# Kernel tuning notes

Hardware: AMD Instinct MI355X
Metric: run time of the kernel (lower is better)

## Reference

```python
import jax, jax.numpy as jnp
import numpy as np

NUM_EXPERTS_TOTAL = 9  # 8 routed + 1 shared (shared expert is also routed via softmax in this module)
TOP_K = 2


def setup_inputs() -> dict:
    key = jax.random.key(0)
    k0, k1, k2, k3, k4 = jax.random.split(key, 5)
    B, S, H, I = 2, 2048, 1024, 2816
    E = NUM_EXPERTS_TOTAL
    x = jax.random.normal(k0, (B, S, H), dtype=jnp.float32)
    Wr = (jax.random.normal(k1, (H, E), dtype=jnp.float32) * 0.02)          # router (no bias)
    Wg = (jax.random.normal(k2, (E, H, I), dtype=jnp.float32) * 0.02)       # gate_proj per expert
    Wu = (jax.random.normal(k3, (E, H, I), dtype=jnp.float32) * 0.02)       # up_proj per expert
    Wd = (jax.random.normal(k4, (E, I, H), dtype=jnp.float32) * 0.02)       # down_proj per expert
    return {"x": x, "Wr": Wr, "Wg": Wg, "Wu": Wu, "Wd": Wd}


def reference(x, Wr, Wg, Wu, Wd):
    B, S, H = x.shape
    E = NUM_EXPERTS_TOTAL
    T = B * S

    # Router: softmax over all 9 experts, then top-2 and renormalize
    logits = jnp.einsum('bsh,he->bse', x, Wr)
    probs = jax.nn.softmax(logits, axis=-1)
    topk_w, topk_idx = jax.lax.top_k(probs, TOP_K)                 # [B,S,K]
    topk_w = topk_w / jnp.sum(topk_w, axis=-1, keepdims=True)

    xf = x.reshape(T, H)
    wf = topk_w.reshape(T, TOP_K)
    idxf = topk_idx.reshape(T, TOP_K)

    # Per-token combine weight for each expert (0 if not selected)
    cw = jnp.zeros((T, E), dtype=x.dtype).at[jnp.arange(T)[:, None], idxf].add(wf)  # [T,E]

    # SwiGLU MLP for every expert (tokens with cw==0 contribute nothing)
    gate = jax.nn.silu(jnp.einsum('th,ehi->tei', xf, Wg))          # [T,E,I]
    hidden = gate * jnp.einsum('th,ehi->tei', xf, Wu)              # [T,E,I]
    out = jnp.einsum('tei,eih,te->th', hidden, Wd, cw)             # weighted combine
    return out.reshape(B, S, H)
```

## Files before the change

kernel.cpp:

```cpp
#include <hip/hip_runtime.h>
#include <cstdint>
#include <cstddef>

#define T_TOK 4096
#define H_DIM 1024
#define I_DIM 2816
#define E_NUM 9
#define MAXTILE 76

typedef __bf16 bf16;
typedef bf16 bf16x4 __attribute__((ext_vector_type(4)));
typedef bf16 bf16x8 __attribute__((ext_vector_type(8)));
typedef float f32x4 __attribute__((ext_vector_type(4)));

constexpr int BM = 128, BN = 128, BK = 32;

#define GL16(gp, lp)                                                                   \
  __builtin_amdgcn_global_load_lds((const __attribute__((address_space(1))) void*)(gp), \
                                   (__attribute__((address_space(3))) void*)(lp), 16, 0, 0)

__global__ __launch_bounds__(256) void k_xcast(const float* __restrict__ x, bf16* __restrict__ xb) {
  size_t i = ((size_t)blockIdx.x * 256 + threadIdx.x) * 8;
  float4 a = *reinterpret_cast<const float4*>(x + i);
  float4 b = *reinterpret_cast<const float4*>(x + i + 4);
  bf16x8 v;
  v[0]=(bf16)a.x; v[1]=(bf16)a.y; v[2]=(bf16)a.z; v[3]=(bf16)a.w;
  v[4]=(bf16)b.x; v[5]=(bf16)b.y; v[6]=(bf16)b.z; v[7]=(bf16)b.w;
  *reinterpret_cast<bf16x8*>(xb + i) = v;
}

__global__ __launch_bounds__(256) void k_transpose(const float* __restrict__ in,
                                                   bf16* __restrict__ out, int R, int C) {
  const float* src = in + (size_t)blockIdx.z * R * C;
  bf16* dst = out + (size_t)blockIdx.z * R * C;
  __shared__ bf16 tile[64][72];
  int r0 = blockIdx.y * 64, c0 = blockIdx.x * 64;
  int t = threadIdx.x;
  int tr = t >> 4, tc = (t & 15) * 4;
#pragma unroll
  for (int it = 0; it < 4; ++it) {
    int r = tr + it * 16;
    float4 v = *reinterpret_cast<const float4*>(src + (size_t)(r0 + r) * C + c0 + tc);
    bf16x4 w; w[0]=(bf16)v.x; w[1]=(bf16)v.y; w[2]=(bf16)v.z; w[3]=(bf16)v.w;
    *reinterpret_cast<bf16x4*>(&tile[r][tc]) = w;
  }
  __syncthreads();
#pragma unroll
  for (int it = 0; it < 4; ++it) {
    int oc = tr + it * 16;
    bf16x4 w;
    w[0] = tile[tc + 0][oc]; w[1] = tile[tc + 1][oc];
    w[2] = tile[tc + 2][oc]; w[3] = tile[tc + 3][oc];
    *reinterpret_cast<bf16x4*>(dst + (size_t)(c0 + oc) * R + r0 + tc) = w;
  }
}

__global__ __launch_bounds__(256) void k_router(const float* __restrict__ x,
                                                const float* __restrict__ Wr,
                                                int* __restrict__ ridx,
                                                float* __restrict__ rw,
                                                int* __restrict__ counts) {
  int lane = threadIdx.x & 63;
  int wid  = threadIdx.x >> 6;
  int t = blockIdx.x * 4 + wid;
  const float* xr = x + (size_t)t * H_DIM;
  float acc[E_NUM];
#pragma unroll
  for (int e = 0; e < E_NUM; ++e) acc[e] = 0.f;
  for (int h = lane; h < H_DIM; h += 64) {
    float xv = xr[h];
    const float* wr = Wr + h * E_NUM;
#pragma unroll
    for (int e = 0; e < E_NUM; ++e) acc[e] += xv * wr[e];
  }
#pragma unroll
  for (int off = 32; off > 0; off >>= 1) {
#pragma unroll
    for (int e = 0; e < E_NUM; ++e) acc[e] += __shfl_xor(acc[e], off);
  }
  if (lane == 0) {
    int i0 = 0;
#pragma unroll
    for (int e = 1; e < E_NUM; ++e) if (acc[e] > acc[i0]) i0 = e;
    int i1 = (i0 == 0) ? 1 : 0;
#pragma unroll
    for (int e = 0; e < E_NUM; ++e) if (e != i0 && acc[e] > acc[i1]) i1 = e;
    float r  = expf(acc[i1] - acc[i0]);
    float w0 = 1.f / (1.f + r);
    float w1 = r / (1.f + r);
    ridx[2 * t]     = i0;
    ridx[2 * t + 1] = i1;
    rw[2 * t]     = w0;
    rw[2 * t + 1] = w1;
    atomicAdd(&counts[i0], 1);
    atomicAdd(&counts[i1], 1);
  }
}

__global__ void k_scan(const int* __restrict__ counts, int* __restrict__ offsets,
                       int* __restrict__ cursor, int* __restrict__ tiles,
                       int* __restrict__ n_tiles) {
  if (threadIdx.x == 0) {
    int s = 0, nt = 0;
    for (int e = 0; e < E_NUM; ++e) {
      offsets[e] = s;
      int c = counts[e];
      for (int pt = 0; pt * BM < c && nt < MAXTILE; ++pt) tiles[nt++] = (e << 16) | pt;
      s += c;
    }
    offsets[E_NUM] = s;
    *n_tiles = nt;
  }
  if (threadIdx.x < E_NUM) cursor[threadIdx.x] = 0;
}

__global__ __launch_bounds__(256) void k_scatter(const int* __restrict__ ridx,
                                                 const int* __restrict__ offsets,
                                                 int* __restrict__ cursor,
                                                 int* __restrict__ perm) {
  int t = blockIdx.x * 256 + threadIdx.x;
  if (t >= T_TOK) return;
#pragma unroll
  for (int k = 0; k < 2; ++k) {
    int e = ridx[2 * t + k];
    int pos = atomicAdd(&cursor[e], 1);
    perm[offsets[e] + pos] = 2 * t + k;
  }
}

__global__ __launch_bounds__(256, 2) void k_gateup(const bf16* __restrict__ xb,
                                                   const bf16* __restrict__ WgT,
                                                   const bf16* __restrict__ WuT,
                                                   const int* __restrict__ perm,
                                                   const int* __restrict__ offsets,
                                                   const int* __restrict__ tiles,
                                                   const int* __restrict__ n_tiles,
                                                   bf16* __restrict__ hidden) {
  if ((int)blockIdx.y >= *n_tiles) return;
  int tv = tiles[blockIdx.y];
  int e = tv >> 16, pt = tv & 0xffff;
  int seg0 = offsets[e], cnt = offsets[e + 1] - seg0;
  int n0 = blockIdx.x * BN;

  __shared__ bf16 As[BM * BK];
  __shared__ bf16 Bg[BN * BK];
  __shared__ bf16 Bu[BN * BK];

  int tid = threadIdx.x, lane = tid & 63, wid = tid >> 6;
  int wm = wid >> 1, wn = wid & 1, l15 = lane & 15, l16 = lane >> 4;

  int srow1 = tid >> 2, srow2 = 64 + (tid >> 2);
  int kc = (tid & 3) * 8;
  int p1 = pt * BM + srow1, p2 = pt * BM + srow2;
  const bf16* a1 = xb + (size_t)(perm[seg0 + (p1 < cnt ? p1 : 0)] >> 1) * H_DIM + kc;
  const bf16* a2 = xb + (size_t)(perm[seg0 + (p2 < cnt ? p2 : 0)] >> 1) * H_DIM + kc;
  const bf16* g1 = WgT + ((size_t)e * I_DIM + n0 + srow1) * H_DIM + kc;
  const bf16* g2 = WgT + ((size_t)e * I_DIM + n0 + srow2) * H_DIM + kc;
  const bf16* u1 = WuT + ((size_t)e * I_DIM + n0 + srow1) * H_DIM + kc;
  const bf16* u2 = WuT + ((size_t)e * I_DIM + n0 + srow2) * H_DIM + kc;
  bf16* lA1 = &As[tid * 8];       bf16* lA2 = &As[2048 + tid * 8];
  bf16* lG1 = &Bg[tid * 8];       bf16* lG2 = &Bg[2048 + tid * 8];
  bf16* lU1 = &Bu[tid * 8];       bf16* lU2 = &Bu[2048 + tid * 8];

  f32x4 accg[4][4], accu[4][4];
#pragma unroll
  for (int m = 0; m < 4; ++m)
#pragma unroll
    for (int n = 0; n < 4; ++n) {
      accg[m][n] = (f32x4){0.f, 0.f, 0.f, 0.f};
      accu[m][n] = (f32x4){0.f, 0.f, 0.f, 0.f};
    }

  for (int k0 = 0; k0 < H_DIM; k0 += BK) {
    GL16(a1 + k0, lA1);  GL16(a2 + k0, lA2);
    GL16(g1 + k0, lG1);  GL16(g2 + k0, lG2);
    GL16(u1 + k0, lU1);  GL16(u2 + k0, lU2);
    __syncthreads();

    bf16x8 af[4], bg[4], bu[4];
#pragma unroll
    for (int m = 0; m < 4; ++m)
      af[m] = *reinterpret_cast<const bf16x8*>(&As[(wm * 64 + m * 16 + l15) * BK + l16 * 8]);
#pragma unroll
    for (int n = 0; n < 4; ++n) {
      bg[n] = *reinterpret_cast<const bf16x8*>(&Bg[(wn * 64 + n * 16 + l15) * BK + l16 * 8]);
      bu[n] = *reinterpret_cast<const bf16x8*>(&Bu[(wn * 64 + n * 16 + l15) * BK + l16 * 8]);
    }
#pragma unroll
    for (int m = 0; m < 4; ++m)
#pragma unroll
      for (int n = 0; n < 4; ++n) {
        accg[m][n] = __builtin_amdgcn_mfma_f32_16x16x32_bf16(af[m], bg[n], accg[m][n], 0, 0, 0);
        accu[m][n] = __builtin_amdgcn_mfma_f32_16x16x32_bf16(af[m], bu[n], accu[m][n], 0, 0, 0);
      }
    __syncthreads();
  }

#pragma unroll
  for (int m = 0; m < 4; ++m) {
#pragma unroll
    for (int r = 0; r < 4; ++r) {
      int p_glob = pt * BM + wm * 64 + m * 16 + l16 * 4 + r;
      if (p_glob < cnt) {
        bf16* hrow = hidden + (size_t)(seg0 + p_glob) * I_DIM;
#pragma unroll
        for (int n = 0; n < 4; ++n) {
          int col = n0 + wn * 64 + n * 16 + l15;
          float g = accg[m][n][r];
          float u = accu[m][n][r];
          float h = g / (1.f + __expf(-g)) * u;
          hrow[col] = (bf16)h;
        }
      }
    }
  }
}

__global__ __launch_bounds__(256, 2) void k_down(const bf16* __restrict__ hidden,
                                                 const bf16* __restrict__ WdT,
                                                 const int* __restrict__ perm,
                                                 const int* __restrict__ offsets,
                                                 const int* __restrict__ tiles,
                                                 const int* __restrict__ n_tiles,
                                                 float* __restrict__ pair_out) {
  if ((int)blockIdx.y >= *n_tiles) return;
  int tv = tiles[blockIdx.y];
  int e = tv >> 16, pt = tv & 0xffff;
  int seg0 = offsets[e], cnt = offsets[e + 1] - seg0;
  int n0 = blockIdx.x * BN;

  __shared__ bf16 As[BM * BK];
  __shared__ bf16 Bs[BN * BK];

  int tid = threadIdx.x, lane = tid & 63, wid = tid >> 6;
  int wm = wid >> 1, wn = wid & 1, l15 = lane & 15, l16 = lane >> 4;

  int srow1 = tid >> 2, srow2 = 64 + (tid >> 2);
  int kc = (tid & 3) * 8;
  int p1 = pt * BM + srow1, p2 = pt * BM + srow2;
  const bf16* a1 = hidden + (size_t)(seg0 + (p1 < cnt ? p1 : 0)) * I_DIM + kc;
  const bf16* a2 = hidden + (size_t)(seg0 + (p2 < cnt ? p2 : 0)) * I_DIM + kc;
  const bf16* b1 = WdT + ((size_t)e * H_DIM + n0 + srow1) * I_DIM + kc;
  const bf16* b2 = WdT + ((size_t)e * H_DIM + n0 + srow2) * I_DIM + kc;
  bf16* lA1 = &As[tid * 8];  bf16* lA2 = &As[2048 + tid * 8];
  bf16* lB1 = &Bs[tid * 8];  bf16* lB2 = &Bs[2048 + tid * 8];

  f32x4 acc[4][4];
#pragma unroll
  for (int m = 0; m < 4; ++m)
#pragma unroll
    for (int n = 0; n < 4; ++n) acc[m][n] = (f32x4){0.f, 0.f, 0.f, 0.f};

  for (int k0 = 0; k0 < I_DIM; k0 += BK) {
    GL16(a1 + k0, lA1);  GL16(a2 + k0, lA2);
    GL16(b1 + k0, lB1);  GL16(b2 + k0, lB2);
    __syncthreads();

    bf16x8 af[4], bfr[4];
#pragma unroll
    for (int m = 0; m < 4; ++m)
      af[m] = *reinterpret_cast<const bf16x8*>(&As[(wm * 64 + m * 16 + l15) * BK + l16 * 8]);
#pragma unroll
    for (int n = 0; n < 4; ++n)
      bfr[n] = *reinterpret_cast<const bf16x8*>(&Bs[(wn * 64 + n * 16 + l15) * BK + l16 * 8]);
#pragma unroll
    for (int m = 0; m < 4; ++m)
#pragma unroll
      for (int n = 0; n < 4; ++n)
        acc[m][n] = __builtin_amdgcn_mfma_f32_16x16x32_bf16(af[m], bfr[n], acc[m][n], 0, 0, 0);
    __syncthreads();
  }

#pragma unroll
  for (int m = 0; m < 4; ++m) {
#pragma unroll
    for (int r = 0; r < 4; ++r) {
      int p_glob = pt * BM + wm * 64 + m * 16 + l16 * 4 + r;
      if (p_glob < cnt) {
        int pair = perm[seg0 + p_glob];
        float* orow = pair_out + (size_t)pair * H_DIM;
#pragma unroll
        for (int n = 0; n < 4; ++n) {
          int col = n0 + wn * 64 + n * 16 + l15;
          orow[col] = acc[m][n][r];
        }
      }
    }
  }
}

__global__ __launch_bounds__(256) void k_combine(const float* __restrict__ pair_out,
                                                 const float* __restrict__ rw,
                                                 float* __restrict__ out) {
  int t = blockIdx.x;
  int c = threadIdx.x;
  float w0 = rw[2 * t];
  float w1 = rw[2 * t + 1];
  float4 a = *reinterpret_cast<const float4*>(pair_out + ((size_t)(2 * t)) * H_DIM + c * 4);
  float4 b = *reinterpret_cast<const float4*>(pair_out + ((size_t)(2 * t + 1)) * H_DIM + c * 4);
  float4 o;
  o.x = w0 * a.x + w1 * b.x;
  o.y = w0 * a.y + w1 * b.y;
  o.z = w0 * a.z + w1 * b.z;
  o.w = w0 * a.w + w1 * b.w;
  *reinterpret_cast<float4*>(out + (size_t)t * H_DIM + c * 4) = o;
}

extern "C" void kernel_launch(void* const* d_in, const int* in_sizes, int n_in,
                              void* d_out, int out_size, void* d_ws, size_t ws_size,
                              hipStream_t stream) {
  const float* x  = (const float*)d_in[0];
  const float* Wr = (const float*)d_in[1];
  const float* Wg = (const float*)d_in[2];
  const float* Wu = (const float*)d_in[3];
  const float* Wd = (const float*)d_in[4];
  float* out = (float*)d_out;

  char* ws = (char*)d_ws;
  int*   counts  = (int*)(ws);
  int*   cursor  = (int*)(ws + 256);
  int*   offsets = (int*)(ws + 512);
  int*   n_tiles = (int*)(ws + 768);
  int*   tiles   = (int*)(ws + 1024);
  int*   ridx    = (int*)(ws + 64 * 1024);
  float* rw      = (float*)(ws + 128 * 1024);
  int*   perm    = (int*)(ws + 192 * 1024);
  bf16*  xb      = (bf16*)(ws + (1ull << 20));
  bf16*  WgT     = (bf16*)(ws + (16ull << 20));
  bf16*  WuT     = (bf16*)(ws + (66ull << 20));
  bf16*  WdT     = (bf16*)(ws + (116ull << 20));
  bf16*  hidden  = (bf16*)(ws + (166ull << 20));
  float* pair_out = (float*)(ws + (212ull << 20));

  hipMemsetAsync(counts, 0, 64, stream);
  k_xcast<<<dim3(T_TOK * H_DIM / 2048), dim3(256), 0, stream>>>(x, xb);
  k_transpose<<<dim3(I_DIM / 64, H_DIM / 64, E_NUM), dim3(256), 0, stream>>>(Wg, WgT, H_DIM, I_DIM);
  k_transpose<<<dim3(I_DIM / 64, H_DIM / 64, E_NUM), dim3(256), 0, stream>>>(Wu, WuT, H_DIM, I_DIM);
  k_transpose<<<dim3(H_DIM / 64, I_DIM / 64, E_NUM), dim3(256), 0, stream>>>(Wd, WdT, I_DIM, H_DIM);
  k_router<<<dim3(T_TOK / 4), dim3(256), 0, stream>>>(x, Wr, ridx, rw, counts);
  k_scan<<<dim3(1), dim3(64), 0, stream>>>(counts, offsets, cursor, tiles, n_tiles);
  k_scatter<<<dim3((T_TOK + 255) / 256), dim3(256), 0, stream>>>(ridx, offsets, cursor, perm);
  k_gateup<<<dim3(I_DIM / BN, MAXTILE), dim3(256), 0, stream>>>(
      xb, WgT, WuT, perm, offsets, tiles, n_tiles, hidden);
  k_down<<<dim3(H_DIM / BN, MAXTILE), dim3(256), 0, stream>>>(
      hidden, WdT, perm, offsets, tiles, n_tiles, pair_out);
  k_combine<<<dim3(T_TOK), dim3(256), 0, stream>>>(pair_out, rw, out);
}
```

Measured before the change: 486.4 us.

## Double-buffer LDS tiles in gate/up and down expert GEMMs

Both grouped GEMM kernels now keep two LDS buffers per operand. The next K-tile's global-to-LDS loads are issued before the MFMA work on the current tile, so memory latency can overlap compute instead of sitting behind a barrier each iteration. The down kernel's launch bounds also rise to 3 blocks per CU to raise occupancy. The cost is double the LDS per block and possible register pressure. Correctness depends on the barrier waiting for the outstanding async LDS loads.

```diff
diff --git a/kernel.cpp b/kernel.cpp
--- a/kernel.cpp
+++ b/kernel.cpp
@@ -142,9 +142,9 @@
   int seg0 = offsets[e], cnt = offsets[e + 1] - seg0;
   int n0 = blockIdx.x * BN;
 
-  __shared__ bf16 As[BM * BK];
-  __shared__ bf16 Bg[BN * BK];
-  __shared__ bf16 Bu[BN * BK];
+  __shared__ bf16 As[2][BM * BK];
+  __shared__ bf16 Bg[2][BN * BK];
+  __shared__ bf16 Bu[2][BN * BK];
 
   int tid = threadIdx.x, lane = tid & 63, wid = tid >> 6;
   int wm = wid >> 1, wn = wid & 1, l15 = lane & 15, l16 = lane >> 4;
@@ -158,9 +158,6 @@
   const bf16* g2 = WgT + ((size_t)e * I_DIM + n0 + srow2) * H_DIM + kc;
   const bf16* u1 = WuT + ((size_t)e * I_DIM + n0 + srow1) * H_DIM + kc;
   const bf16* u2 = WuT + ((size_t)e * I_DIM + n0 + srow2) * H_DIM + kc;
-  bf16* lA1 = &As[tid * 8];       bf16* lA2 = &As[2048 + tid * 8];
-  bf16* lG1 = &Bg[tid * 8];       bf16* lG2 = &Bg[2048 + tid * 8];
-  bf16* lU1 = &Bu[tid * 8];       bf16* lU2 = &Bu[2048 + tid * 8];
 
   f32x4 accg[4][4], accu[4][4];
 #pragma unroll
@@ -171,20 +168,21 @@
       accu[m][n] = (f32x4){0.f, 0.f, 0.f, 0.f};
     }
 
-  for (int k0 = 0; k0 < H_DIM; k0 += BK) {
-    GL16(a1 + k0, lA1);  GL16(a2 + k0, lA2);
-    GL16(g1 + k0, lG1);  GL16(g2 + k0, lG2);
-    GL16(u1 + k0, lU1);  GL16(u2 + k0, lU2);
-    __syncthreads();
-
+  auto STAGE = [&](int b, int kt) {
+    int k0 = kt * BK;
+    GL16(a1 + k0, &As[b][tid * 8]);  GL16(a2 + k0, &As[b][2048 + tid * 8]);
+    GL16(g1 + k0, &Bg[b][tid * 8]);  GL16(g2 + k0, &Bg[b][2048 + tid * 8]);
+    GL16(u1 + k0, &Bu[b][tid * 8]);  GL16(u2 + k0, &Bu[b][2048 + tid * 8]);
+  };
+  auto COMPUTE = [&](int b) {
     bf16x8 af[4], bg[4], bu[4];
 #pragma unroll
     for (int m = 0; m < 4; ++m)
-      af[m] = *reinterpret_cast<const bf16x8*>(&As[(wm * 64 + m * 16 + l15) * BK + l16 * 8]);
+      af[m] = *reinterpret_cast<const bf16x8*>(&As[b][(wm * 64 + m * 16 + l15) * BK + l16 * 8]);
 #pragma unroll
     for (int n = 0; n < 4; ++n) {
-      bg[n] = *reinterpret_cast<const bf16x8*>(&Bg[(wn * 64 + n * 16 + l15) * BK + l16 * 8]);
-      bu[n] = *reinterpret_cast<const bf16x8*>(&Bu[(wn * 64 + n * 16 + l15) * BK + l16 * 8]);
+      bg[n] = *reinterpret_cast<const bf16x8*>(&Bg[b][(wn * 64 + n * 16 + l15) * BK + l16 * 8]);
+      bu[n] = *reinterpret_cast<const bf16x8*>(&Bu[b][(wn * 64 + n * 16 + l15) * BK + l16 * 8]);
     }
 #pragma unroll
     for (int m = 0; m < 4; ++m)
@@ -193,6 +191,17 @@
         accg[m][n] = __builtin_amdgcn_mfma_f32_16x16x32_bf16(af[m], bg[n], accg[m][n], 0, 0, 0);
         accu[m][n] = __builtin_amdgcn_mfma_f32_16x16x32_bf16(af[m], bu[n], accu[m][n], 0, 0, 0);
       }
+  };
+
+  constexpr int NT = H_DIM / BK;
+  STAGE(0, 0);
+  __syncthreads();
+  for (int kt = 0; kt < NT; kt += 2) {
+    if (kt + 1 < NT) STAGE(1, kt + 1);
+    COMPUTE(0);
+    __syncthreads();
+    if (kt + 2 < NT) STAGE(0, kt + 2);
+    COMPUTE(1);
     __syncthreads();
   }
 
@@ -216,7 +225,7 @@
   }
 }
 
-__global__ __launch_bounds__(256, 2) void k_down(const bf16* __restrict__ hidden,
+__global__ __launch_bounds__(256, 3) void k_down(const bf16* __restrict__ hidden,
                                                  const bf16* __restrict__ WdT,
                                                  const int* __restrict__ perm,
                                                  const int* __restrict__ offsets,
@@ -229,8 +238,8 @@
   int seg0 = offsets[e], cnt = offsets[e + 1] - seg0;
   int n0 = blockIdx.x * BN;
 
-  __shared__ bf16 As[BM * BK];
-  __shared__ bf16 Bs[BN * BK];
+  __shared__ bf16 As[2][BM * BK];
+  __shared__ bf16 Bs[2][BN * BK];
 
   int tid = threadIdx.x, lane = tid & 63, wid = tid >> 6;
   int wm = wid >> 1, wn = wid & 1, l15 = lane & 15, l16 = lane >> 4;
@@ -242,8 +251,6 @@
   const bf16* a2 = hidden + (size_t)(seg0 + (p2 < cnt ? p2 : 0)) * I_DIM + kc;
   const bf16* b1 = WdT + ((size_t)e * H_DIM + n0 + srow1) * I_DIM + kc;
   const bf16* b2 = WdT + ((size_t)e * H_DIM + n0 + srow2) * I_DIM + kc;
-  bf16* lA1 = &As[tid * 8];  bf16* lA2 = &As[2048 + tid * 8];
-  bf16* lB1 = &Bs[tid * 8];  bf16* lB2 = &Bs[2048 + tid * 8];
 
   f32x4 acc[4][4];
 #pragma unroll
@@ -251,23 +258,35 @@
 #pragma unroll
     for (int n = 0; n < 4; ++n) acc[m][n] = (f32x4){0.f, 0.f, 0.f, 0.f};
 
-  for (int k0 = 0; k0 < I_DIM; k0 += BK) {
-    GL16(a1 + k0, lA1);  GL16(a2 + k0, lA2);
-    GL16(b1 + k0, lB1);  GL16(b2 + k0, lB2);
-    __syncthreads();
-
+  auto STAGE = [&](int b, int kt) {
+    int k0 = kt * BK;
+    GL16(a1 + k0, &As[b][tid * 8]);  GL16(a2 + k0, &As[b][2048 + tid * 8]);
+    GL16(b1 + k0, &Bs[b][tid * 8]);  GL16(b2 + k0, &Bs[b][2048 + tid * 8]);
+  };
+  auto COMPUTE = [&](int b) {
     bf16x8 af[4], bfr[4];
 #pragma unroll
     for (int m = 0; m < 4; ++m)
-      af[m] = *reinterpret_cast<const bf16x8*>(&As[(wm * 64 + m * 16 + l15) * BK + l16 * 8]);
+      af[m] = *reinterpret_cast<const bf16x8*>(&As[b][(wm * 64 + m * 16 + l15) * BK + l16 * 8]);
 #pragma unroll
     for (int n = 0; n < 4; ++n)
-      bfr[n] = *reinterpret_cast<const bf16x8*>(&Bs[(wn * 64 + n * 16 + l15) * BK + l16 * 8]);
+      bfr[n] = *reinterpret_cast<const bf16x8*>(&Bs[b][(wn * 64 + n * 16 + l15) * BK + l16 * 8]);
 #pragma unroll
     for (int m = 0; m < 4; ++m)
 #pragma unroll
       for (int n = 0; n < 4; ++n)
         acc[m][n] = __builtin_amdgcn_mfma_f32_16x16x32_bf16(af[m], bfr[n], acc[m][n], 0, 0, 0);
+  };
+
+  constexpr int NT = I_DIM / BK;
+  STAGE(0, 0);
+  __syncthreads();
+  for (int kt = 0; kt < NT; kt += 2) {
+    if (kt + 1 < NT) STAGE(1, kt + 1);
+    COMPUTE(0);
+    __syncthreads();
+    if (kt + 2 < NT) STAGE(0, kt + 2);
+    COMPUTE(1);
     __syncthreads();
   }
 
```

Measured after the change: 504.6 us. 3.7% more time.

## Swizzle LDS tiles and split-K the down projection with atomic accumulation

Applied to the files above, without the earlier changes.

XOR-swizzles the 16-byte k-chunk position by row in both expert GEMM kernels so that fragment reads from LDS avoid bank conflicts. It also splits the down-projection reduction over I into two halves via a z grid dimension, which doubles the block count for the small-N down GEMM. Partial sums are accumulated into pair_out with float atomics, so a memset of pair_out is added. The cost is extra atomic traffic, a 32 MB zeroing pass, and a summation order that is no longer deterministic.

```diff
diff --git a/kernel.cpp b/kernel.cpp
--- a/kernel.cpp
+++ b/kernel.cpp
@@ -149,8 +149,8 @@
   int tid = threadIdx.x, lane = tid & 63, wid = tid >> 6;
   int wm = wid >> 1, wn = wid & 1, l15 = lane & 15, l16 = lane >> 4;
 
-  int srow1 = tid >> 2, srow2 = 64 + (tid >> 2);
-  int kc = (tid & 3) * 8;
+  int srow1 = tid >> 2, srow2 = 64 + srow1;
+  int kc = (((tid & 3) ^ (srow1 & 3)) * 8);
   int p1 = pt * BM + srow1, p2 = pt * BM + srow2;
   const bf16* a1 = xb + (size_t)(perm[seg0 + (p1 < cnt ? p1 : 0)] >> 1) * H_DIM + kc;
   const bf16* a2 = xb + (size_t)(perm[seg0 + (p2 < cnt ? p2 : 0)] >> 1) * H_DIM + kc;
@@ -162,6 +162,8 @@
   bf16* lG1 = &Bg[tid * 8];       bf16* lG2 = &Bg[2048 + tid * 8];
   bf16* lU1 = &Bu[tid * 8];       bf16* lU2 = &Bu[2048 + tid * 8];
 
+  int rsl = (l16 ^ (l15 & 3)) * 8;
+
   f32x4 accg[4][4], accu[4][4];
 #pragma unroll
   for (int m = 0; m < 4; ++m)
@@ -180,11 +182,11 @@
     bf16x8 af[4], bg[4], bu[4];
 #pragma unroll
     for (int m = 0; m < 4; ++m)
-      af[m] = *reinterpret_cast<const bf16x8*>(&As[(wm * 64 + m * 16 + l15) * BK + l16 * 8]);
+      af[m] = *reinterpret_cast<const bf16x8*>(&As[(wm * 64 + m * 16 + l15) * BK + rsl]);
 #pragma unroll
     for (int n = 0; n < 4; ++n) {
-      bg[n] = *reinterpret_cast<const bf16x8*>(&Bg[(wn * 64 + n * 16 + l15) * BK + l16 * 8]);
-      bu[n] = *reinterpret_cast<const bf16x8*>(&Bu[(wn * 64 + n * 16 + l15) * BK + l16 * 8]);
+      bg[n] = *reinterpret_cast<const bf16x8*>(&Bg[(wn * 64 + n * 16 + l15) * BK + rsl]);
+      bu[n] = *reinterpret_cast<const bf16x8*>(&Bu[(wn * 64 + n * 16 + l15) * BK + rsl]);
     }
 #pragma unroll
     for (int m = 0; m < 4; ++m)
@@ -228,6 +230,7 @@
   int e = tv >> 16, pt = tv & 0xffff;
   int seg0 = offsets[e], cnt = offsets[e + 1] - seg0;
   int n0 = blockIdx.x * BN;
+  int kz = blockIdx.z * (I_DIM / 2);
 
   __shared__ bf16 As[BM * BK];
   __shared__ bf16 Bs[BN * BK];
@@ -235,23 +238,25 @@
   int tid = threadIdx.x, lane = tid & 63, wid = tid >> 6;
   int wm = wid >> 1, wn = wid & 1, l15 = lane & 15, l16 = lane >> 4;
 
-  int srow1 = tid >> 2, srow2 = 64 + (tid >> 2);
-  int kc = (tid & 3) * 8;
+  int srow1 = tid >> 2, srow2 = 64 + srow1;
+  int kc = (((tid & 3) ^ (srow1 & 3)) * 8);
   int p1 = pt * BM + srow1, p2 = pt * BM + srow2;
-  const bf16* a1 = hidden + (size_t)(seg0 + (p1 < cnt ? p1 : 0)) * I_DIM + kc;
-  const bf16* a2 = hidden + (size_t)(seg0 + (p2 < cnt ? p2 : 0)) * I_DIM + kc;
-  const bf16* b1 = WdT + ((size_t)e * H_DIM + n0 + srow1) * I_DIM + kc;
-  const bf16* b2 = WdT + ((size_t)e * H_DIM + n0 + srow2) * I_DIM + kc;
+  const bf16* a1 = hidden + (size_t)(seg0 + (p1 < cnt ? p1 : 0)) * I_DIM + kz + kc;
+  const bf16* a2 = hidden + (size_t)(seg0 + (p2 < cnt ? p2 : 0)) * I_DIM + kz + kc;
+  const bf16* b1 = WdT + ((size_t)e * H_DIM + n0 + srow1) * I_DIM + kz + kc;
+  const bf16* b2 = WdT + ((size_t)e * H_DIM + n0 + srow2) * I_DIM + kz + kc;
   bf16* lA1 = &As[tid * 8];  bf16* lA2 = &As[2048 + tid * 8];
   bf16* lB1 = &Bs[tid * 8];  bf16* lB2 = &Bs[2048 + tid * 8];
 
+  int rsl = (l16 ^ (l15 & 3)) * 8;
+
   f32x4 acc[4][4];
 #pragma unroll
   for (int m = 0; m < 4; ++m)
 #pragma unroll
     for (int n = 0; n < 4; ++n) acc[m][n] = (f32x4){0.f, 0.f, 0.f, 0.f};
 
-  for (int k0 = 0; k0 < I_DIM; k0 += BK) {
+  for (int k0 = 0; k0 < I_DIM / 2; k0 += BK) {
     GL16(a1 + k0, lA1);  GL16(a2 + k0, lA2);
     GL16(b1 + k0, lB1);  GL16(b2 + k0, lB2);
     __syncthreads();
@@ -259,10 +264,10 @@
     bf16x8 af[4], bfr[4];
 #pragma unroll
     for (int m = 0; m < 4; ++m)
-      af[m] = *reinterpret_cast<const bf16x8*>(&As[(wm * 64 + m * 16 + l15) * BK + l16 * 8]);
+      af[m] = *reinterpret_cast<const bf16x8*>(&As[(wm * 64 + m * 16 + l15) * BK + rsl]);
 #pragma unroll
     for (int n = 0; n < 4; ++n)
-      bfr[n] = *reinterpret_cast<const bf16x8*>(&Bs[(wn * 64 + n * 16 + l15) * BK + l16 * 8]);
+      bfr[n] = *reinterpret_cast<const bf16x8*>(&Bs[(wn * 64 + n * 16 + l15) * BK + rsl]);
 #pragma unroll
     for (int m = 0; m < 4; ++m)
 #pragma unroll
@@ -282,7 +287,7 @@
 #pragma unroll
         for (int n = 0; n < 4; ++n) {
           int col = n0 + wn * 64 + n * 16 + l15;
-          orow[col] = acc[m][n][r];
+          atomicAdd(&orow[col], acc[m][n][r]);
         }
       }
     }
@@ -333,6 +338,7 @@
   float* pair_out = (float*)(ws + (212ull << 20));
 
   hipMemsetAsync(counts, 0, 64, stream);
+  hipMemsetAsync(pair_out, 0, (size_t)2 * T_TOK * H_DIM * sizeof(float), stream);
   k_xcast<<<dim3(T_TOK * H_DIM / 2048), dim3(256), 0, stream>>>(x, xb);
   k_transpose<<<dim3(I_DIM / 64, H_DIM / 64, E_NUM), dim3(256), 0, stream>>>(Wg, WgT, H_DIM, I_DIM);
   k_transpose<<<dim3(I_DIM / 64, H_DIM / 64, E_NUM), dim3(256), 0, stream>>>(Wu, WuT, H_DIM, I_DIM);
@@ -342,7 +348,7 @@
   k_scatter<<<dim3((T_TOK + 255) / 256), dim3(256), 0, stream>>>(ridx, offsets, cursor, perm);
   k_gateup<<<dim3(I_DIM / BN, MAXTILE), dim3(256), 0, stream>>>(
       xb, WgT, WuT, perm, offsets, tiles, n_tiles, hidden);
-  k_down<<<dim3(H_DIM / BN, MAXTILE), dim3(256), 0, stream>>>(
+  k_down<<<dim3(H_DIM / BN, MAXTILE, 2), dim3(256), 0, stream>>>(
       hidden, WdT, perm, offsets, tiles, n_tiles, pair_out);
   k_combine<<<dim3(T_TOK), dim3(256), 0, stream>>>(pair_out, rw, out);
 }
```

Result: slower. 537.5 us (+10.5%).

## Replace weight transposes with 8x8 blockified bf16 layout and raise occupancy hint

Applied to the files above, without the earlier changes.

Replaces the shared-memory tiled transpose of the expert weights with a register-only blockify kernel. It writes the weights as contiguous 8(k)x8(n) bf16 blocks, and the GEMM kernels' global-to-LDS loads are re-indexed to read that layout. The goal is a cheaper weight preprocessing pass, since there is no LDS round trip and reads and writes are fully coalesced. Launch bounds for both GEMMs are raised from 2 to 4 blocks per CU, which may restrict registers for the 32-accumulator gate/up kernel and cause spills. Each weight-load slot now strides across k-rows I_DIM*8 apart, which changes the access pattern the GEMMs see.

```diff
diff --git a/kernel.cpp b/kernel.cpp
--- a/kernel.cpp
+++ b/kernel.cpp
@@ -9,7 +9,6 @@
 #define MAXTILE 76
 
 typedef __bf16 bf16;
-typedef bf16 bf16x4 __attribute__((ext_vector_type(4)));
 typedef bf16 bf16x8 __attribute__((ext_vector_type(8)));
 typedef float f32x4 __attribute__((ext_vector_type(4)));
 
@@ -29,29 +28,31 @@
   *reinterpret_cast<bf16x8*>(xb + i) = v;
 }
 
-__global__ __launch_bounds__(256) void k_transpose(const float* __restrict__ in,
-                                                   bf16* __restrict__ out, int R, int C) {
-  const float* src = in + (size_t)blockIdx.z * R * C;
-  bf16* dst = out + (size_t)blockIdx.z * R * C;
-  __shared__ bf16 tile[64][72];
-  int r0 = blockIdx.y * 64, c0 = blockIdx.x * 64;
-  int t = threadIdx.x;
-  int tr = t >> 4, tc = (t & 15) * 4;
-#pragma unroll
-  for (int it = 0; it < 4; ++it) {
-    int r = tr + it * 16;
-    float4 v = *reinterpret_cast<const float4*>(src + (size_t)(r0 + r) * C + c0 + tc);
-    bf16x4 w; w[0]=(bf16)v.x; w[1]=(bf16)v.y; w[2]=(bf16)v.z; w[3]=(bf16)v.w;
-    *reinterpret_cast<bf16x4*>(&tile[r][tc]) = w;
-  }
-  __syncthreads();
-#pragma unroll
-  for (int it = 0; it < 4; ++it) {
-    int oc = tr + it * 16;
-    bf16x4 w;
-    w[0] = tile[tc + 0][oc]; w[1] = tile[tc + 1][oc];
-    w[2] = tile[tc + 2][oc]; w[3] = tile[tc + 3][oc];
-    *reinterpret_cast<bf16x4*>(dst + (size_t)(c0 + oc) * R + r0 + tc) = w;
+__global__ __launch_bounds__(256) void k_blockify(const float* __restrict__ in,
+                                                  bf16* __restrict__ out, int R, int C) {
+  const float* src = in + (size_t)blockIdx.y * R * C;
+  bf16* dst = out + (size_t)blockIdx.y * R * C;
+  int flat = blockIdx.x * 256 + threadIdx.x;
+  int CG = C >> 3;
+  int cg = flat % CG;
+  int rb = flat / CG;
+  int c0 = cg * 8;
+  size_t r0 = (size_t)rb * 8;
+  float t[8][8];
+#pragma unroll
+  for (int j = 0; j < 8; ++j) {
+    float4 v0 = *reinterpret_cast<const float4*>(src + (r0 + j) * C + c0);
+    float4 v1 = *reinterpret_cast<const float4*>(src + (r0 + j) * C + c0 + 4);
+    t[j][0]=v0.x; t[j][1]=v0.y; t[j][2]=v0.z; t[j][3]=v0.w;
+    t[j][4]=v1.x; t[j][5]=v1.y; t[j][6]=v1.z; t[j][7]=v1.w;
+  }
+  bf16* d = dst + ((size_t)rb * C + c0) * 8;
+#pragma unroll
+  for (int ii = 0; ii < 8; ++ii) {
+    bf16x8 o;
+#pragma unroll
+    for (int il = 0; il < 8; ++il) o[il] = (bf16)t[il][ii];
+    *reinterpret_cast<bf16x8*>(d + ii * 8) = o;
   }
 }
 
@@ -128,9 +129,9 @@
   }
 }
 
-__global__ __launch_bounds__(256, 2) void k_gateup(const bf16* __restrict__ xb,
-                                                   const bf16* __restrict__ WgT,
-                                                   const bf16* __restrict__ WuT,
+__global__ __launch_bounds__(256, 4) void k_gateup(const bf16* __restrict__ xb,
+                                                   const bf16* __restrict__ Wgb,
+                                                   const bf16* __restrict__ Wub,
                                                    const int* __restrict__ perm,
                                                    const int* __restrict__ offsets,
                                                    const int* __restrict__ tiles,
@@ -149,15 +150,15 @@
   int tid = threadIdx.x, lane = tid & 63, wid = tid >> 6;
   int wm = wid >> 1, wn = wid & 1, l15 = lane & 15, l16 = lane >> 4;
 
-  int srow1 = tid >> 2, srow2 = 64 + (tid >> 2);
-  int kc = (tid & 3) * 8;
+  int srow1 = tid >> 2, srow2 = 64 + srow1;
+  int slot = tid & 3;
   int p1 = pt * BM + srow1, p2 = pt * BM + srow2;
-  const bf16* a1 = xb + (size_t)(perm[seg0 + (p1 < cnt ? p1 : 0)] >> 1) * H_DIM + kc;
-  const bf16* a2 = xb + (size_t)(perm[seg0 + (p2 < cnt ? p2 : 0)] >> 1) * H_DIM + kc;
-  const bf16* g1 = WgT + ((size_t)e * I_DIM + n0 + srow1) * H_DIM + kc;
-  const bf16* g2 = WgT + ((size_t)e * I_DIM + n0 + srow2) * H_DIM + kc;
-  const bf16* u1 = WuT + ((size_t)e * I_DIM + n0 + srow1) * H_DIM + kc;
-  const bf16* u2 = WuT + ((size_t)e * I_DIM + n0 + srow2) * H_DIM + kc;
+  const bf16* a1 = xb + (size_t)(perm[seg0 + (p1 < cnt ? p1 : 0)] >> 1) * H_DIM + slot * 8;
+  const bf16* a2 = xb + (size_t)(perm[seg0 + (p2 < cnt ? p2 : 0)] >> 1) * H_DIM + slot * 8;
+  const bf16* g1 = Wgb + (size_t)e * H_DIM * I_DIM + ((size_t)slot * I_DIM + n0 + srow1) * 8;
+  const bf16* g2 = Wgb + (size_t)e * H_DIM * I_DIM + ((size_t)slot * I_DIM + n0 + srow2) * 8;
+  const bf16* u1 = Wub + (size_t)e * H_DIM * I_DIM + ((size_t)slot * I_DIM + n0 + srow1) * 8;
+  const bf16* u2 = Wub + (size_t)e * H_DIM * I_DIM + ((size_t)slot * I_DIM + n0 + srow2) * 8;
   bf16* lA1 = &As[tid * 8];       bf16* lA2 = &As[2048 + tid * 8];
   bf16* lG1 = &Bg[tid * 8];       bf16* lG2 = &Bg[2048 + tid * 8];
   bf16* lU1 = &Bu[tid * 8];       bf16* lU2 = &Bu[2048 + tid * 8];
@@ -172,9 +173,10 @@
     }
 
   for (int k0 = 0; k0 < H_DIM; k0 += BK) {
+    size_t wk = (size_t)k0 * I_DIM;
     GL16(a1 + k0, lA1);  GL16(a2 + k0, lA2);
-    GL16(g1 + k0, lG1);  GL16(g2 + k0, lG2);
-    GL16(u1 + k0, lU1);  GL16(u2 + k0, lU2);
+    GL16(g1 + wk, lG1);  GL16(g2 + wk, lG2);
+    GL16(u1 + wk, lU1);  GL16(u2 + wk, lU2);
     __syncthreads();
 
     bf16x8 af[4], bg[4], bu[4];
@@ -216,8 +218,8 @@
   }
 }
 
-__global__ __launch_bounds__(256, 2) void k_down(const bf16* __restrict__ hidden,
-                                                 const bf16* __restrict__ WdT,
+__global__ __launch_bounds__(256, 4) void k_down(const bf16* __restrict__ hidden,
+                                                 const bf16* __restrict__ Wdb,
                                                  const int* __restrict__ perm,
                                                  const int* __restrict__ offsets,
                                                  const int* __restrict__ tiles,
@@ -235,13 +237,13 @@
   int tid = threadIdx.x, lane = tid & 63, wid = tid >> 6;
   int wm = wid >> 1, wn = wid & 1, l15 = lane & 15, l16 = lane >> 4;
 
-  int srow1 = tid >> 2, srow2 = 64 + (tid >> 2);
-  int kc = (tid & 3) * 8;
+  int srow1 = tid >> 2, srow2 = 64 + srow1;
+  int slot = tid & 3;
   int p1 = pt * BM + srow1, p2 = pt * BM + srow2;
-  const bf16* a1 = hidden + (size_t)(seg0 + (p1 < cnt ? p1 : 0)) * I_DIM + kc;
-  const bf16* a2 = hidden + (size_t)(seg0 + (p2 < cnt ? p2 : 0)) * I_DIM + kc;
-  const bf16* b1 = WdT + ((size_t)e * H_DIM + n0 + srow1) * I_DIM + kc;
-  const bf16* b2 = WdT + ((size_t)e * H_DIM + n0 + srow2) * I_DIM + kc;
+  const bf16* a1 = hidden + (size_t)(seg0 + (p1 < cnt ? p1 : 0)) * I_DIM + slot * 8;
+  const bf16* a2 = hidden + (size_t)(seg0 + (p2 < cnt ? p2 : 0)) * I_DIM + slot * 8;
+  const bf16* b1 = Wdb + (size_t)e * I_DIM * H_DIM + ((size_t)slot * H_DIM + n0 + srow1) * 8;
+  const bf16* b2 = Wdb + (size_t)e * I_DIM * H_DIM + ((size_t)slot * H_DIM + n0 + srow2) * 8;
   bf16* lA1 = &As[tid * 8];  bf16* lA2 = &As[2048 + tid * 8];
   bf16* lB1 = &Bs[tid * 8];  bf16* lB2 = &Bs[2048 + tid * 8];
 
@@ -252,8 +254,9 @@
     for (int n = 0; n < 4; ++n) acc[m][n] = (f32x4){0.f, 0.f, 0.f, 0.f};
 
   for (int k0 = 0; k0 < I_DIM; k0 += BK) {
+    size_t wk = (size_t)k0 * H_DIM;
     GL16(a1 + k0, lA1);  GL16(a2 + k0, lA2);
-    GL16(b1 + k0, lB1);  GL16(b2 + k0, lB2);
+    GL16(b1 + wk, lB1);  GL16(b2 + wk, lB2);
     __syncthreads();
 
     bf16x8 af[4], bfr[4];
@@ -326,23 +329,25 @@
   float* rw      = (float*)(ws + 128 * 1024);
   int*   perm    = (int*)(ws + 192 * 1024);
   bf16*  xb      = (bf16*)(ws + (1ull << 20));
-  bf16*  WgT     = (bf16*)(ws + (16ull << 20));
-  bf16*  WuT     = (bf16*)(ws + (66ull << 20));
-  bf16*  WdT     = (bf16*)(ws + (116ull << 20));
+  bf16*  Wgb     = (bf16*)(ws + (16ull << 20));
+  bf16*  Wub     = (bf16*)(ws + (66ull << 20));
+  bf16*  Wdb     = (bf16*)(ws + (116ull << 20));
   bf16*  hidden  = (bf16*)(ws + (166ull << 20));
   float* pair_out = (float*)(ws + (212ull << 20));
 
+  constexpr int BLK_BLOCKS = 176;
+
   hipMemsetAsync(counts, 0, 64, stream);
   k_xcast<<<dim3(T_TOK * H_DIM / 2048), dim3(256), 0, stream>>>(x, xb);
-  k_transpose<<<dim3(I_DIM / 64, H_DIM / 64, E_NUM), dim3(256), 0, stream>>>(Wg, WgT, H_DIM, I_DIM);
-  k_transpose<<<dim3(I_DIM / 64, H_DIM / 64, E_NUM), dim3(256), 0, stream>>>(Wu, WuT, H_DIM, I_DIM);
-  k_transpose<<<dim3(H_DIM / 64, I_DIM / 64, E_NUM), dim3(256), 0, stream>>>(Wd, WdT, I_DIM, H_DIM);
+  k_blockify<<<dim3(BLK_BLOCKS, E_NUM), dim3(256), 0, stream>>>(Wg, Wgb, H_DIM, I_DIM);
+  k_blockify<<<dim3(BLK_BLOCKS, E_NUM), dim3(256), 0, stream>>>(Wu, Wub, H_DIM, I_DIM);
+  k_blockify<<<dim3(BLK_BLOCKS, E_NUM), dim3(256), 0, stream>>>(Wd, Wdb, I_DIM, H_DIM);
   k_router<<<dim3(T_TOK / 4), dim3(256), 0, stream>>>(x, Wr, ridx, rw, counts);
   k_scan<<<dim3(1), dim3(64), 0, stream>>>(counts, offsets, cursor, tiles, n_tiles);
   k_scatter<<<dim3((T_TOK + 255) / 256), dim3(256), 0, stream>>>(ridx, offsets, cursor, perm);
   k_gateup<<<dim3(I_DIM / BN, MAXTILE), dim3(256), 0, stream>>>(
-      xb, WgT, WuT, perm, offsets, tiles, n_tiles, hidden);
+      xb, Wgb, Wub, perm, offsets, tiles, n_tiles, hidden);
   k_down<<<dim3(H_DIM / BN, MAXTILE), dim3(256), 0, stream>>>(
-      hidden, WdT, perm, offsets, tiles, n_tiles, pair_out);
+      hidden, Wdb, perm, offsets, tiles, n_tiles, pair_out);
   k_combine<<<dim3(T_TOK), dim3(256), 0, stream>>>(pair_out, rw, out);
 }
```

New measurement: 1.364 ms. 2.8x slower.
